# Performance work log

Measured on AMD Instinct MI355X. Metric: run time of the kernel, lower is better.

Reference implementation:

```python
import math
import jax, jax.numpy as jnp
import numpy as np

NB_HEADS = 32
NB_KV_HEADS = 8
HEAD_DIM = 64
ROPE_THETA = 10000.0


def _rope_modulator(seq_len, dim, theta):
    # (seq_len, dim//2, 2): (cos, sin) of 2*pi*t / theta^(2k/d)  -- note nonstandard 2*pi factor
    freqs = 1.0 / theta ** (jnp.arange(0, dim - 1, 2, dtype=jnp.float32) / dim)
    t = jnp.arange(seq_len, dtype=jnp.float32) * (2.0 * math.pi)
    angles = t[:, None] * freqs[None, :]
    return jnp.stack((jnp.cos(angles), jnp.sin(angles)), axis=-1)


def _apply_rope(qk, rm):
    # qk: (B, H, S, hd); pairs are consecutive (even, odd) lanes
    B, H, S, hd = qk.shape
    qk = qk.reshape(B, H, S, hd // 2, 2)
    c, s = rm[:S, :, 0], rm[:S, :, 1]  # (S, hd//2)
    re = qk[..., 0] * c - qk[..., 1] * s
    im = qk[..., 0] * s + qk[..., 1] * c
    return jnp.stack((re, im), axis=-1).reshape(B, H, S, hd)


def setup_inputs() -> dict:
    key = jax.random.key(0)
    k1, k2, k3, k4, k5 = jax.random.split(key, 5)
    D = NB_HEADS * HEAD_DIM  # 2048
    Dkv = NB_KV_HEADS * HEAD_DIM  # 512
    std = D ** -0.5
    return {
        "x": jax.random.normal(k1, (2, 2048, D), dtype=jnp.float32),
        "Wq": jax.random.normal(k2, (D, D), dtype=jnp.float32) * std,
        "Wk": jax.random.normal(k3, (Dkv, D), dtype=jnp.float32) * std,
        "Wv": jax.random.normal(k4, (Dkv, D), dtype=jnp.float32) * std,
        "Wo": jax.random.normal(k5, (D, D), dtype=jnp.float32) * std,
    }


def reference(x, Wq, Wk, Wv, Wo):
    B, S, D = x.shape
    g = NB_HEADS // NB_KV_HEADS
    rm = _rope_modulator(S, HEAD_DIM, ROPE_THETA)

    q = (x @ Wq.T).reshape(B, S, NB_HEADS, HEAD_DIM).transpose(0, 2, 1, 3)
    k = (x @ Wk.T).reshape(B, S, NB_KV_HEADS, HEAD_DIM).transpose(0, 2, 1, 3)
    v = (x @ Wv.T).reshape(B, S, NB_KV_HEADS, HEAD_DIM).transpose(0, 2, 1, 3)

    q = _apply_rope(q, rm)
    k = _apply_rope(k, rm)

    # GQA: expand KV heads (repeat_interleave over head dim)
    k = jnp.repeat(k, g, axis=1)  # (B, H, S, hd)
    v = jnp.repeat(v, g, axis=1)

    scale = 1.0 / math.sqrt(HEAD_DIM)
    scores = jnp.einsum("bhqd,bhkd->bhqk", q, k) * scale
    causal = jnp.tril(jnp.ones((S, S), dtype=bool))
    scores = jnp.where(causal, scores, jnp.finfo(scores.dtype).min)
    attn = jax.nn.softmax(scores, axis=-1)
    z = jnp.einsum("bhqk,bhkd->bhqd", attn, v)  # (B, H, S, hd)
    z = z.transpose(0, 2, 1, 3).reshape(B, S, D)
    return z @ Wo.T
```

## Files before the change

kernel.cpp:

```cpp
#include <hip/hip_runtime.h>
#include <hip/hip_bf16.h>
#include <math.h>

#define B_   2
#define S_   2048
#define H_   32
#define HKV_ 8
#define HD_  64
#define D_   2048
#define DKV_ 512
#define M_   (B_*S_)

typedef __attribute__((ext_vector_type(8))) short bf16x8;
typedef __attribute__((ext_vector_type(4))) float f32x4;
typedef __attribute__((ext_vector_type(16))) float f32x16;
typedef unsigned short u16;

__device__ __forceinline__ u16 f2bf(float f) {
    union { float f; unsigned u; } v; v.f = f;
    unsigned r = v.u + 0x7fff + ((v.u >> 16) & 1);
    return (u16)(r >> 16);
}

__device__ __forceinline__ unsigned cvt_pk_bf16(float lo, float hi) {
    unsigned r;
    asm("v_cvt_pk_bf16_f32 %0, %1, %2" : "=v"(r) : "v"(lo), "v"(hi));
    return r;
}
__device__ __forceinline__ void perm32swap(unsigned &a, unsigned &b) {
    asm volatile("v_permlane32_swap_b32 %0, %1" : "+v"(a), "+v"(b));
}

typedef __attribute__((address_space(3))) void lds_void;
typedef const __attribute__((address_space(1))) void g_void;
__device__ __forceinline__ void gl_lds16(const void* g, void* l) {
    __builtin_amdgcn_global_load_lds((g_void*)g, (lds_void*)l, 16, 0, 0);
}

__global__ void rope_table_kernel(float* __restrict__ tab) {
    int idx = blockIdx.x * blockDim.x + threadIdx.x;
    int s = idx >> 5, i = idx & 31;
    double freq = pow(10000.0, -(double)i / 32.0);
    double ang = (double)s * 6.283185307179586476925286766559 * freq;
    tab[2*idx]   = (float)cos(ang);
    tab[2*idx+1] = (float)sin(ang);
}

__global__ void cvt_all_kernel(const float* __restrict__ x,  const float* __restrict__ wq,
                               const float* __restrict__ wk, const float* __restrict__ wv,
                               u16* __restrict__ xb, u16* __restrict__ wall) {
    int i = blockIdx.x * blockDim.x + threadIdx.x;
    if (i >= 1835008) return;
    const float* src; u16* dst;
    size_t e = (size_t)i * 8;
    if (i < 1048576)      { src = x  + e;            dst = xb + e; }
    else if (i < 1572864) { src = wq + (e - 8388608);  dst = wall + (e - 8388608); }
    else if (i < 1703936) { src = wk + (e - 12582912); dst = wall + 4194304 + (e - 12582912); }
    else                  { src = wv + (e - 13631488); dst = wall + 5242880 + (e - 13631488); }
    float4 a = *(const float4*)src;
    float4 b = *(const float4*)(src + 4);
    u16 tmp[8] = {f2bf(a.x), f2bf(a.y), f2bf(a.z), f2bf(a.w),
                  f2bf(b.x), f2bf(b.y), f2bf(b.z), f2bf(b.w)};
    *(uint4*)dst = *(const uint4*)tmp;
}

__global__ void cvt_bf16_kernel(const float* __restrict__ src, u16* __restrict__ dst, int n8) {
    int i = blockIdx.x * blockDim.x + threadIdx.x;
    if (i >= n8) return;
    const float4* p = (const float4*)(src + (size_t)i * 8);
    float4 a = p[0], b = p[1];
    u16 tmp[8] = {f2bf(a.x), f2bf(a.y), f2bf(a.z), f2bf(a.w),
                  f2bf(b.x), f2bf(b.y), f2bf(b.z), f2bf(b.w)};
    *(uint4*)(dst + (size_t)i * 8) = *(const uint4*)tmp;
}

template<bool YF32, bool ROPE>
__launch_bounds__(256, 2)
__global__ void gemm_bt_bf16(const u16* __restrict__ X, const u16* __restrict__ W,
                             void* __restrict__ Y, const float2* __restrict__ tab,
                             int Ndim, int Kdim) {
    __shared__ u16 As[128*32];
    __shared__ u16 Bs[128*32];
    int tid = threadIdx.x;
    int wv = tid >> 6, lane = tid & 63;
    int quad = lane >> 4, lr = lane & 15;
    int wm = wv >> 1, wn = wv & 1;
    int m0 = blockIdx.y * 128, n0 = blockIdx.x * 128;

    int srow = wv*32 + (lane >> 2);
    int scol = (lane & 3) * 8;
    const u16* xp = X + (size_t)(m0 + srow)*Kdim + scol;
    const u16* wp = W + (size_t)(n0 + srow)*Kdim + scol;

    f32x4 acc[4][4] = {};
    for (int k0 = 0; k0 < Kdim; k0 += 32) {
        __syncthreads();
        gl_lds16(xp + k0,                   &As[wv*1024]);
        gl_lds16(xp + 16*(size_t)Kdim + k0, &As[wv*1024 + 512]);
        gl_lds16(wp + k0,                   &Bs[wv*1024]);
        gl_lds16(wp + 16*(size_t)Kdim + k0, &Bs[wv*1024 + 512]);
        __syncthreads();
        bf16x8 af[4], bfr[4];
        #pragma unroll
        for (int t = 0; t < 4; ++t) {
            af[t]  = *(const bf16x8*)(&As[(wm*64 + t*16 + lr)*32 + quad*8]);
            bfr[t] = *(const bf16x8*)(&Bs[(wn*64 + t*16 + lr)*32 + quad*8]);
        }
        #pragma unroll
        for (int mt = 0; mt < 4; ++mt)
            #pragma unroll
            for (int nt = 0; nt < 4; ++nt)
                acc[mt][nt] = __builtin_amdgcn_mfma_f32_16x16x32_bf16(af[mt], bfr[nt], acc[mt][nt], 0, 0, 0);
    }
    #pragma unroll
    for (int mt = 0; mt < 4; ++mt)
        #pragma unroll
        for (int nt = 0; nt < 4; ++nt)
            #pragma unroll
            for (int r = 0; r < 4; ++r) {
                int m = m0 + wm*64 + mt*16 + quad*4 + r;
                int n = n0 + wn*64 + nt*16 + lr;
                float val = acc[mt][nt][r];
                if constexpr (ROPE) {
                    float partner = __shfl_xor(val, 1);
                    if (n < 2560) {
                        float2 cs = tab[(size_t)(m & (S_-1))*32 + ((n >> 1) & 31)];
                        val = fmaf(cs.x, val, ((n & 1) ? cs.y : -cs.y) * partner);
                    }
                }
                if constexpr (YF32)
                    ((float*)Y)[(size_t)m*Ndim + n] = val;
                else
                    ((u16*)Y)[(size_t)m*Ndim + n] = f2bf(val);
            }
}

#define LDK 40
template<bool F32>
__device__ __forceinline__ void stage8(const void* src, u16* dst, size_t row, int col, int ld) {
    if constexpr (F32) {
        const float* p = (const float*)src + row * (size_t)ld + col;
        float4 a = *(const float4*)p;
        float4 b = *(const float4*)(p + 4);
        u16 tmp[8] = {f2bf(a.x), f2bf(a.y), f2bf(a.z), f2bf(a.w),
                      f2bf(b.x), f2bf(b.y), f2bf(b.z), f2bf(b.w)};
        *(uint4*)dst = *(const uint4*)tmp;
    } else {
        const u16* p = (const u16*)src + row * (size_t)ld + col;
        *(uint4*)dst = *(const uint4*)p;
    }
}

template<bool XF32, bool WF32, bool YF32, bool ROPE>
__launch_bounds__(256, 2)
__global__ void gemm_bt(const void* __restrict__ X, const void* __restrict__ W,
                        void* __restrict__ Y, const float2* __restrict__ tab,
                        int Ndim, int Kdim) {
    __shared__ u16 As[128*LDK];
    __shared__ u16 Bs[128*LDK];
    int tid = threadIdx.x;
    int wv = tid >> 6, lane = tid & 63;
    int quad = lane >> 4, lr = lane & 15;
    int wm = wv >> 1, wn = wv & 1;
    int m0 = blockIdx.y * 128, n0 = blockIdx.x * 128;

    f32x4 acc[4][4] = {};
    for (int k0 = 0; k0 < Kdim; k0 += 32) {
        __syncthreads();
        #pragma unroll
        for (int it = 0; it < 2; ++it) {
            int e = (it*256 + tid) * 8;
            int r = e >> 5, kk = e & 31;
            stage8<XF32>(X, &As[r*LDK + kk], (size_t)(m0 + r), k0 + kk, Kdim);
            stage8<WF32>(W, &Bs[r*LDK + kk], (size_t)(n0 + r), k0 + kk, Kdim);
        }
        __syncthreads();
        bf16x8 af[4], bfr[4];
        #pragma unroll
        for (int t = 0; t < 4; ++t) {
            af[t]  = *(const bf16x8*)(&As[(wm*64 + t*16 + lr)*LDK + quad*8]);
            bfr[t] = *(const bf16x8*)(&Bs[(wn*64 + t*16 + lr)*LDK + quad*8]);
        }
        #pragma unroll
        for (int mt = 0; mt < 4; ++mt)
            #pragma unroll
            for (int nt = 0; nt < 4; ++nt)
                acc[mt][nt] = __builtin_amdgcn_mfma_f32_16x16x32_bf16(af[mt], bfr[nt], acc[mt][nt], 0, 0, 0);
    }
    #pragma unroll
    for (int mt = 0; mt < 4; ++mt)
        #pragma unroll
        for (int nt = 0; nt < 4; ++nt)
            #pragma unroll
            for (int r = 0; r < 4; ++r) {
                int m = m0 + wm*64 + mt*16 + quad*4 + r;
                int n = n0 + wn*64 + nt*16 + lr;
                float val = acc[mt][nt][r];
                if constexpr (ROPE) {
                    float partner = __shfl_xor(val, 1);
                    if (n < 2560) {
                        float2 cs = tab[(size_t)(m & (S_-1))*32 + ((n >> 1) & 31)];
                        val = fmaf(cs.x, val, ((n & 1) ? cs.y : -cs.y) * partner);
                    }
                }
                if constexpr (YF32)
                    ((float*)Y)[(size_t)m*Ndim + n] = val;
                else
                    ((u16*)Y)[(size_t)m*Ndim + n] = f2bf(val);
            }
}

__launch_bounds__(256, 4)
__global__ void attn_kernel(const u16* __restrict__ qkv, u16* __restrict__ z) {
    __shared__ u16 Ks[2][64*64];
    __shared__ u16 Vt[2][64*64];
    int tid = threadIdx.x;
    int wv = tid >> 6, lane = tid & 63;
    int qcol = lane & 31, hi = lane >> 5;
    int id = blockIdx.x;
    int qt = 15 - (id >> 6);
    int bh = id & 63;
    int h = bh >> 1, b = bh & 1;
    int kvh = h >> 2;
    int qrow_base = qt*128 + wv*32;
    int jmax = 2*qt + 1;

    const u16* qkvb = qkv + (size_t)(b*S_) * 3072;
    const u16* kbase = qkvb + 2048 + kvh*64;

    int kr = lane >> 3;
    int dcs = lane & 7;
    int sg = tid & 7;
    int sp = tid >> 3;
    const u16* vbase = qkvb + 2560 + kvh*64 + sg*8;

    #pragma unroll
    for (int i = 0; i < 2; ++i) {
        int c = 2*wv + i;
        int kvloc = c*8 + kr;
        int dc = dcs ^ ((kvloc + (kvloc >> 3)) & 7);
        gl_lds16(kbase + (size_t)kvloc*3072 + dc*8, &Ks[0][c*512]);
    }
    uint4 vr0 = *(const uint4*)(vbase + (size_t)(2*sp)*3072);
    uint4 vr1 = *(const uint4*)(vbase + (size_t)(2*sp + 1)*3072);

    bf16x8 bq[4];
    {
        const u16* qp = qkvb + (size_t)(qrow_base + qcol)*3072 + h*64 + hi*8;
        #pragma unroll
        for (int ds = 0; ds < 4; ++ds)
            bq[ds] = *(const bf16x8*)(qp + ds*16);
    }

    f32x16 oacc[2] = {};
    float lsum = 0.f;
    const float SC = 0.18033688f;

    for (int j = 0; j <= jmax; ++j) {
        int buf = j & 1;
        {
            const u16* a0 = (const u16*)&vr0;
            const u16* a1 = (const u16*)&vr1;
            #pragma unroll
            for (int jx = 0; jx < 8; ++jx) {
                unsigned pk = (unsigned)a0[jx] | ((unsigned)a1[jx] << 16);
                int kvs = (2*sp) ^ (8*(jx ^ sg));
                *(unsigned*)(&Vt[buf][(sg*8 + jx)*64 + kvs]) = pk;
            }
        }
        __syncthreads();

        if (j < jmax) {
            int kvn = (j+1)*64;
            #pragma unroll
            for (int i = 0; i < 2; ++i) {
                int c = 2*wv + i;
                int kvloc = c*8 + kr;
                int dc = dcs ^ ((kvloc + (kvloc >> 3)) & 7);
                gl_lds16(kbase + (size_t)(kvn + kvloc)*3072 + dc*8, &Ks[buf^1][c*512]);
            }
            vr0 = *(const uint4*)(vbase + (size_t)(kvn + 2*sp)*3072);
            vr1 = *(const uint4*)(vbase + (size_t)(kvn + 2*sp + 1)*3072);
        }

        int kv0 = j*64;
        if (kv0 < qrow_base + 32) {
            #pragma unroll
            for (int t = 0; t < 2; ++t) {
                int kvt = kv0 + t*32;
                if (kvt <= qrow_base + 31) {
                    f32x16 sacc = {};
                    int krow = t*32 + qcol;
                    int ksw = (krow + (krow >> 3)) & 7;
                    #pragma unroll
                    for (int ds = 0; ds < 4; ++ds) {
                        bf16x8 ak = *(const bf16x8*)(&Ks[buf][krow*64 + (((2*ds + hi) ^ ksw)*8)]);
                        sacc = __builtin_amdgcn_mfma_f32_32x32x16_bf16(ak, bq[ds], sacc, 0, 0, 0);
                    }
                    float p[16];
                    if (kvt + 31 > qrow_base) {
                        #pragma unroll
                        for (int r = 0; r < 16; ++r) {
                            int kvg = kvt + (r & 3) + 8*(r >> 2) + 4*hi;
                            float pv = exp2f(fmaf(sacc[r], SC, -4.0f));
                            if (kvg > qrow_base + qcol) pv = 0.f;
                            p[r] = pv; lsum += pv;
                        }
                    } else {
                        #pragma unroll
                        for (int r = 0; r < 16; ++r) {
                            p[r] = exp2f(fmaf(sacc[r], SC, -4.0f));
                            lsum += p[r];
                        }
                    }
                    unsigned U0[4], U1[4];
                    #pragma unroll
                    for (int g = 0; g < 4; ++g) {
                        U0[g] = cvt_pk_bf16(p[4*g],     p[4*g + 1]);
                        U1[g] = cvt_pk_bf16(p[4*g + 2], p[4*g + 3]);
                    }
                    #pragma unroll
                    for (int s = 0; s < 2; ++s) {
                        unsigned w0 = U0[2*s], w2 = U0[2*s + 1];
                        unsigned w1 = U1[2*s], w3 = U1[2*s + 1];
                        perm32swap(w0, w2);
                        perm32swap(w1, w3);
                        uint4 paw; paw.x = w0; paw.y = w1; paw.z = w2; paw.w = w3;
                        bf16x8 pa = __builtin_bit_cast(bf16x8, paw);
                        #pragma unroll
                        for (int dt = 0; dt < 2; ++dt) {
                            int d = dt*32 + qcol;
                            int g8 = (d & 7) ^ ((d >> 3) & 7);
                            int lc = 4*t + 2*s + hi;
                            bf16x8 bv = *(const bf16x8*)(&Vt[buf][d*64 + ((lc ^ g8)*8)]);
                            oacc[dt] = __builtin_amdgcn_mfma_f32_32x32x16_bf16(pa, bv, oacc[dt], 0, 0, 0);
                        }
                    }
                }
            }
        }
    }

    lsum += __shfl_xor(lsum, 32);
    __syncthreads();
    float* Lb = (float*)&Ks[0][0];
    if (hi == 0) Lb[wv*32 + qcol] = lsum;
    __syncthreads();

    #pragma unroll
    for (int r = 0; r < 16; ++r) {
        int crow = (r & 3) + 8*(r >> 2) + 4*hi;
        int row = qrow_base + crow;
        float li = Lb[wv*32 + crow];
        #pragma unroll
        for (int dt = 0; dt < 2; ++dt)
            z[(size_t)(b*S_ + row)*D_ + h*64 + dt*32 + qcol] = f2bf(oacc[dt][r] / li);
    }
}

extern "C" void kernel_launch(void* const* d_in, const int* in_sizes, int n_in,
                              void* d_out, int out_size, void* d_ws, size_t ws_size,
                              hipStream_t stream) {
    const float* x  = (const float*)d_in[0];
    const float* Wq = (const float*)d_in[1];
    const float* Wk = (const float*)d_in[2];
    const float* Wv = (const float*)d_in[3];
    const float* Wo = (const float*)d_in[4];
    float* out = (float*)d_out;
    char* ws = (char*)d_ws;

    const size_t OFF_XB   = 0;
    const size_t OFF_WALL = 16777216;
    const size_t OFF_TAB  = 29360128;
    const size_t OFF_QKV  = 29884416;
    const size_t NEED     = 55050240;

    float*  tab  = (float*)(ws + OFF_TAB);
    float2* tab2 = (float2*)(ws + OFF_TAB);

    if (ws_size >= NEED) {
        u16* xb   = (u16*)(ws + OFF_XB);
        u16* wall = (u16*)(ws + OFF_WALL);
        u16* qkv  = (u16*)(ws + OFF_QKV);
        u16* zbuf = (u16*)(ws + OFF_XB);
        u16* wob  = (u16*)(ws + 16777216);

        rope_table_kernel<<<256, 256, 0, stream>>>(tab);
        cvt_all_kernel<<<7168, 256, 0, stream>>>(x, Wq, Wk, Wv, xb, wall);
        gemm_bt_bf16<false, true><<<dim3(24, 32), 256, 0, stream>>>(xb, wall, qkv, tab2, 3072, 2048);
        cvt_bf16_kernel<<<2048, 256, 0, stream>>>(Wo, wob, D_*D_/8);
        attn_kernel<<<1024, 256, 0, stream>>>(qkv, zbuf);
        gemm_bt_bf16<true, false><<<dim3(16, 32), 256, 0, stream>>>(zbuf, wob, out, tab2, 2048, 2048);
    } else {
        u16* qkv  = (u16*)(ws + 524288);
        u16* zbuf = (u16*)(ws + 524288 + (size_t)M_*3072*2);

        rope_table_kernel<<<256, 256, 0, stream>>>(tab);
        gemm_bt<true, true, false, true ><<<dim3(16, 32), 256, 0, stream>>>(x, Wq, qkv,        tab2, 3072, 2048);
        gemm_bt<true, true, false, true ><<<dim3(4,  32), 256, 0, stream>>>(x, Wk, qkv + 2048, tab2, 3072, 2048);
        gemm_bt<true, true, false, false><<<dim3(4,  32), 256, 0, stream>>>(x, Wv, qkv + 2560, tab2, 3072, 2048);
        attn_kernel<<<1024, 256, 0, stream>>>(qkv, zbuf);
        gemm_bt<false, true, true, false><<<dim3(16, 32), 256, 0, stream>>>(zbuf, Wo, out, tab2, 2048, 2048);
    }
}
```

Baseline: 301.9 us.

## Add 256x256 eight-wave pipelined GEMM kernel for the fused QKV projection

Adds a new bf16 GEMM kernel with 256x256 tiles, 512 threads, and double-buffered 64-wide K tiles in LDS. Each iteration runs eight phases that interleave direct global-to-LDS loads with MFMA compute, using XOR-swizzled LDS addressing, s_setprio, and explicit waitcnt/barrier control. It replaces the 128x128 kernel for the QKV projection only. The goal is more data reuse per tile and better overlap of memory and compute. In exchange it uses about 128KB of LDS per block, needs a more fragile hand-written schedule, and launches fewer blocks (192), which may underfill the GPU.

```diff
diff --git a/kernel.cpp b/kernel.cpp
--- a/kernel.cpp
+++ b/kernel.cpp
@@ -74,6 +74,122 @@
     *(uint4*)(dst + (size_t)i * 8) = *(const uint4*)tmp;
 }
 
+#define GPH(BI, MH, NH, SB, SA, SH, KT, WEND) do {                                         \
+    bf16x8 af_[4][2], bf_[2][2];                                                           \
+    _Pragma("unroll")                                                                      \
+    for (int mtl = 0; mtl < 4; ++mtl)                                                      \
+        _Pragma("unroll")                                                                  \
+        for (int kk = 0; kk < 2; ++kk)                                                     \
+            af_[mtl][kk] = *(const bf16x8*)(&As[BI][((MH)*128 + wm*64 + mtl*16 + lr)*64 + (((kk*4+quad)^sw)*8)]); \
+    _Pragma("unroll")                                                                      \
+    for (int ntl = 0; ntl < 2; ++ntl)                                                      \
+        _Pragma("unroll")                                                                  \
+        for (int kk = 0; kk < 2; ++kk)                                                     \
+            bf_[ntl][kk] = *(const bf16x8*)(&Bs[BI][((NH)*128 + wn*32 + ntl*16 + lr)*64 + (((kk*4+quad)^sw)*8)]); \
+    { int k0s_ = (KT) << 6;                                                                \
+      int sr_ = (SH)*128 + wvid*16;                                                        \
+      if (SA) { gl_lds16(xsrc + (size_t)sr_*Kdim + k0s_,     &As[SB][sr_*64]);             \
+                gl_lds16(xsrc + (size_t)(sr_+8)*Kdim + k0s_, &As[SB][(sr_+8)*64]); }       \
+      else    { gl_lds16(wsrc + (size_t)sr_*Kdim + k0s_,     &Bs[SB][sr_*64]);             \
+                gl_lds16(wsrc + (size_t)(sr_+8)*Kdim + k0s_, &Bs[SB][(sr_+8)*64]); } }     \
+    __builtin_amdgcn_s_barrier();                                                          \
+    asm volatile("s_waitcnt lgkmcnt(0)" ::: "memory");                                     \
+    __builtin_amdgcn_sched_barrier(0);                                                     \
+    __builtin_amdgcn_s_setprio(1);                                                         \
+    _Pragma("unroll")                                                                      \
+    for (int mtl = 0; mtl < 4; ++mtl)                                                      \
+        _Pragma("unroll")                                                                  \
+        for (int ntl = 0; ntl < 2; ++ntl) {                                                \
+            acc[MH][NH][mtl][ntl] = __builtin_amdgcn_mfma_f32_16x16x32_bf16(af_[mtl][0], bf_[ntl][0], acc[MH][NH][mtl][ntl], 0, 0, 0); \
+            acc[MH][NH][mtl][ntl] = __builtin_amdgcn_mfma_f32_16x16x32_bf16(af_[mtl][1], bf_[ntl][1], acc[MH][NH][mtl][ntl], 0, 0, 0); \
+        }                                                                                  \
+    __builtin_amdgcn_s_setprio(0);                                                         \
+    if (WEND) asm volatile("s_waitcnt vmcnt(4)" ::: "memory");                             \
+    __builtin_amdgcn_s_barrier();                                                          \
+} while (0)
+
+template<bool YF32, bool ROPE>
+__launch_bounds__(512, 2)
+__global__ void gemm_bt_8p(const u16* __restrict__ X, const u16* __restrict__ W,
+                           void* __restrict__ Y, const float2* __restrict__ tab,
+                           int Ndim, int Kdim) {
+    __shared__ u16 As[2][256*64];
+    __shared__ u16 Bs[2][256*64];
+    int tid = threadIdx.x;
+    int wvid = tid >> 6, lane = tid & 63;
+    int quad = lane >> 4, lr = lane & 15;
+    int wm = wvid >> 2, wn = wvid & 3;
+    int m0 = blockIdx.y * 256, n0 = blockIdx.x * 256;
+    int sw = lr & 7;
+
+    int lgr = lane >> 3, lch = lane & 7;
+    size_t goff = (size_t)lgr * Kdim + (size_t)((lch ^ lgr) * 8);
+    const u16* xsrc = X + (size_t)m0 * Kdim + goff;
+    const u16* wsrc = W + (size_t)n0 * Kdim + goff;
+
+    int NT64 = Kdim >> 6;
+
+    {
+        int r0 = wvid*16;
+        gl_lds16(xsrc + (size_t)r0*Kdim,             &As[0][r0*64]);
+        gl_lds16(xsrc + (size_t)(r0+8)*Kdim,         &As[0][(r0+8)*64]);
+        gl_lds16(wsrc + (size_t)(128+r0)*Kdim,       &Bs[0][(128+r0)*64]);
+        gl_lds16(wsrc + (size_t)(128+r0+8)*Kdim,     &Bs[0][(128+r0+8)*64]);
+        gl_lds16(xsrc + (size_t)(128+r0)*Kdim,       &As[0][(128+r0)*64]);
+        gl_lds16(xsrc + (size_t)(128+r0+8)*Kdim,     &As[0][(128+r0+8)*64]);
+        gl_lds16(wsrc + (size_t)r0*Kdim,             &Bs[0][r0*64]);
+        gl_lds16(wsrc + (size_t)(r0+8)*Kdim,         &Bs[0][(r0+8)*64]);
+        gl_lds16(xsrc + (size_t)r0*Kdim + 64,        &As[1][r0*64]);
+        gl_lds16(xsrc + (size_t)(r0+8)*Kdim + 64,    &As[1][(r0+8)*64]);
+        gl_lds16(wsrc + (size_t)(128+r0)*Kdim + 64,  &Bs[1][(128+r0)*64]);
+        gl_lds16(wsrc + (size_t)(128+r0+8)*Kdim + 64,&Bs[1][(128+r0+8)*64]);
+    }
+    asm volatile("s_waitcnt vmcnt(4)" ::: "memory");
+    __builtin_amdgcn_s_barrier();
+
+    f32x4 acc[2][2][4][2] = {};
+    int NTI = NT64 >> 1;
+    for (int t = 0; t < NTI; ++t) {
+        int kt1 = 2*t + 1;
+        int kt2 = (2*t + 2 < NT64) ? (2*t + 2) : 0;
+        int kt3 = (2*t + 3 < NT64) ? (2*t + 3) : 0;
+        GPH(0, 0,0, 1,1,1, kt1, 0);
+        GPH(0, 0,1, 1,0,0, kt1, 0);
+        GPH(0, 1,1, 0,1,0, kt2, 0);
+        GPH(0, 1,0, 0,0,1, kt2, 1);
+        GPH(1, 0,0, 0,1,1, kt2, 0);
+        GPH(1, 0,1, 0,0,0, kt2, 0);
+        GPH(1, 1,1, 1,1,0, kt3, 0);
+        GPH(1, 1,0, 1,0,1, kt3, 1);
+    }
+
+    #pragma unroll
+    for (int MH = 0; MH < 2; ++MH)
+        #pragma unroll
+        for (int NH = 0; NH < 2; ++NH)
+            #pragma unroll
+            for (int mt = 0; mt < 4; ++mt)
+                #pragma unroll
+                for (int nt = 0; nt < 2; ++nt)
+                    #pragma unroll
+                    for (int r = 0; r < 4; ++r) {
+                        int m = m0 + MH*128 + wm*64 + mt*16 + quad*4 + r;
+                        int n = n0 + NH*128 + wn*32 + nt*16 + lr;
+                        float val = acc[MH][NH][mt][nt][r];
+                        if constexpr (ROPE) {
+                            float partner = __shfl_xor(val, 1);
+                            if (n < 2560) {
+                                float2 cs = tab[(size_t)(m & (S_-1))*32 + ((n >> 1) & 31)];
+                                val = fmaf(cs.x, val, ((n & 1) ? cs.y : -cs.y) * partner);
+                            }
+                        }
+                        if constexpr (YF32)
+                            ((float*)Y)[(size_t)m*Ndim + n] = val;
+                        else
+                            ((u16*)Y)[(size_t)m*Ndim + n] = f2bf(val);
+                    }
+}
+
 template<bool YF32, bool ROPE>
 __launch_bounds__(256, 2)
 __global__ void gemm_bt_bf16(const u16* __restrict__ X, const u16* __restrict__ W,
@@ -387,7 +503,7 @@
 
         rope_table_kernel<<<256, 256, 0, stream>>>(tab);
         cvt_all_kernel<<<7168, 256, 0, stream>>>(x, Wq, Wk, Wv, xb, wall);
-        gemm_bt_bf16<false, true><<<dim3(24, 32), 256, 0, stream>>>(xb, wall, qkv, tab2, 3072, 2048);
+        gemm_bt_8p<false, true><<<dim3(12, 16), 512, 0, stream>>>(xb, wall, qkv, tab2, 3072, 2048);
         cvt_bf16_kernel<<<2048, 256, 0, stream>>>(Wo, wob, D_*D_/8);
         attn_kernel<<<1024, 256, 0, stream>>>(qkv, zbuf);
         gemm_bt_bf16<true, false><<<dim3(16, 32), 256, 0, stream>>>(zbuf, wob, out, tab2, 2048, 2048);
```

Result: slower. 334.2 us (+10.7%).
